# Performance work log

Hardware: AMD Instinct MI355X
Metric: run time of the kernel (lower is better)

Reference implementation:

```python
import jax, jax.numpy as jnp
import numpy as np

B, NQ = 4, 4096
HF, WF = 96, 96          # single-level feature map -> Nv = 9216
NV = HF * WF
E = 768                  # dim * num_frames = 192 * 4
NH, NP, NL = 8, 4, 1
HD = E // NH             # 96
EPS = 1e-6


def _layer_norm(x, w, b):
    m = jnp.mean(x, axis=-1, keepdims=True)
    v = jnp.var(x, axis=-1, keepdims=True)
    return (x - m) * jax.lax.rsqrt(v + EPS) * w + b


def _msda_core(value, shapes, loc, aw):
    # value: (B, Nv, H, D); loc: (B, Nq, H, L, P, 2) normalized in [0,1];
    # aw: (B, Nq, H, L, P). Bilinear sampling matching F.grid_sample
    # (align_corners=False, padding_mode='zeros'): pixel = loc * size - 0.5.
    Bn, Nv, H, D = value.shape
    Nq, P = loc.shape[1], loc.shape[4]
    out = jnp.zeros((Bn, H, Nq, D), value.dtype)
    start = 0
    for lvl in range(shapes.shape[0]):
        Hl, Wl = int(shapes[lvl, 0]), int(shapes[lvl, 1])
        v = value[:, start:start + Hl * Wl].transpose(0, 2, 1, 3)  # (B,H,S,D)
        start += Hl * Wl
        x = loc[:, :, :, lvl, :, 0] * Wl - 0.5  # (B,Nq,H,P)
        y = loc[:, :, :, lvl, :, 1] * Hl - 0.5
        x0, y0 = jnp.floor(x), jnp.floor(y)
        sampled = jnp.zeros((Bn, H, Nq, P, D), value.dtype)
        for dx in (0, 1):
            for dy in (0, 1):
                xi, yi = x0 + dx, y0 + dy
                w = (1.0 - jnp.abs(x - xi)) * (1.0 - jnp.abs(y - yi))
                valid = (xi >= 0) & (xi <= Wl - 1) & (yi >= 0) & (yi <= Hl - 1)
                idx = (jnp.clip(yi, 0, Hl - 1) * Wl
                       + jnp.clip(xi, 0, Wl - 1)).astype(jnp.int32)
                idx = idx.transpose(0, 2, 1, 3).reshape(Bn, H, Nq * P)
                g = jnp.take_along_axis(v, idx[..., None], axis=2)
                g = g.reshape(Bn, H, Nq, P, D)
                wz = jnp.where(valid, w, 0.0).transpose(0, 2, 1, 3)[..., None]
                sampled = sampled + g * wz
        awl = aw[:, :, :, lvl].transpose(0, 2, 1, 3)[..., None]  # (B,H,Nq,P,1)
        out = out + jnp.sum(sampled * awl, axis=3)
    return out.transpose(0, 2, 1, 3).reshape(Bn, Nq, H * D)


def setup_inputs():
    key = jax.random.key(0)
    ks = jax.random.split(key, 12)
    s = 0.02
    return {
        "query": jax.random.normal(ks[0], (B, NQ, E), jnp.float32),
        "reference_points": jax.random.uniform(ks[1], (B, NQ, NL, 2), jnp.float32),
        "feat": jax.random.normal(ks[2], (B, NV, E), jnp.float32),
        "spatial_shapes": jnp.array([[HF, WF]], jnp.int32),
        "level_start_index": jnp.zeros((NL,), jnp.int32),
        "ln_q_w": jnp.ones((E,), jnp.float32),
        "ln_q_b": jnp.zeros((E,), jnp.float32),
        "ln_f_w": jnp.ones((E,), jnp.float32),
        "ln_f_b": jnp.zeros((E,), jnp.float32),
        "W_value": jax.random.normal(ks[3], (E, E), jnp.float32) * s,
        "b_value": jnp.zeros((E,), jnp.float32),
        "W_off": jax.random.normal(ks[4], (E, NH * NL * NP * 2), jnp.float32) * s,
        "b_off": jax.random.normal(ks[5], (NH * NL * NP * 2,), jnp.float32) * s,
        "W_attn": jax.random.normal(ks[6], (E, NH * NL * NP), jnp.float32) * s,
        "b_attn": jnp.zeros((NH * NL * NP,), jnp.float32),
        "W_out": jax.random.normal(ks[7], (E, E), jnp.float32) * s,
        "b_out": jnp.zeros((E,), jnp.float32),
        "gamma": jax.random.normal(ks[8], (E,), jnp.float32) * s,
    }


def reference(query, reference_points, feat, spatial_shapes, level_start_index,
              ln_q_w, ln_q_b, ln_f_w, ln_f_b, W_value, b_value, W_off, b_off,
              W_attn, b_attn, W_out, b_out, gamma):
    shapes = np.asarray(spatial_shapes)  # static level shapes
    Bn, Nq, _ = query.shape
    Nv = feat.shape[1]
    q = _layer_norm(query, ln_q_w, ln_q_b)
    f = _layer_norm(feat, ln_f_w, ln_f_b)
    value = (f @ W_value + b_value).reshape(Bn, Nv, NH, HD)
    offsets = (q @ W_off + b_off).reshape(Bn, Nq, NH, NL, NP, 2)
    aw = jax.nn.softmax((q @ W_attn + b_attn).reshape(Bn, Nq, NH, NL * NP), -1)
    aw = aw.reshape(Bn, Nq, NH, NL, NP)
    # offset_normalizer = [W_l, H_l] per level
    norm = jnp.stack([jnp.asarray(shapes[:, 1], jnp.float32),
                      jnp.asarray(shapes[:, 0], jnp.float32)], axis=-1)  # (L,2)
    loc = (reference_points[:, :, None, :, None, :]
           + offsets / norm[None, None, None, :, None, :])
    out = _msda_core(value, shapes, loc, aw)
    out = out @ W_out + b_out
    attn = q + out  # mmcv MSDeformAttn adds identity (dropout=eval no-op)
    return query + gamma * attn
```

## Files before the change

### kernel.cpp

```cpp
#include <hip/hip_runtime.h>

#define BB     4
#define NQS    4096
#define NVS    9216
#define E_DIM  768
#define NHEAD  8
#define NPTS   4
#define HDIM   96
#define HFEAT  96
#define WFEAT  96
#define MQR    16384
#define NLNB   13312
#define NTRB   1152
#define NVALB  432
#define OROWS  64

typedef __attribute__((ext_vector_type(8))) short  s8v;
typedef __attribute__((ext_vector_type(4))) short  s4v;
typedef __attribute__((ext_vector_type(4))) float  f4v;

__device__ __forceinline__ unsigned short f2bf(float x) {
    unsigned int u = __builtin_bit_cast(unsigned int, x);
    unsigned int r = (u + 0x7fffu + ((u >> 16) & 1u)) >> 16;
    return (unsigned short)r;
}
__device__ __forceinline__ float bf2f(unsigned short s) {
    unsigned int u = ((unsigned int)s) << 16;
    return __builtin_bit_cast(float, u);
}
__device__ __forceinline__ float bf2f_s(short s) {
    return bf2f((unsigned short)s);
}

#define GLD16(gp, lp) \
    __builtin_amdgcn_global_load_lds( \
        (__attribute__((address_space(1))) void*)(gp), \
        (__attribute__((address_space(3))) void*)(lp), 16, 0, 0)

__global__ __launch_bounds__(256) void prep_kernel(
    const float* __restrict__ q, const float* __restrict__ f,
    const float* __restrict__ qw, const float* __restrict__ qb,
    const float* __restrict__ fw, const float* __restrict__ fb,
    unsigned short* __restrict__ qout, unsigned short* __restrict__ fout,
    float* __restrict__ stats,
    const float* __restrict__ W0, const float* __restrict__ W1,
    unsigned short* __restrict__ T0, unsigned short* __restrict__ T1,
    const float* __restrict__ W_off, const float* __restrict__ W_attn,
    const float* __restrict__ b_off, const float* __restrict__ b_attn,
    unsigned short* __restrict__ Wqc, float* __restrict__ bcat) {
    __shared__ float tile[32][33];
    const int bid = blockIdx.x;

    if (bid < NLNB) {
        const int wv = threadIdx.x >> 6, lane = threadIdx.x & 63;
        const int row = bid * 4 + wv;
        const bool isq = row < MQR;
        const float* x = isq ? (q + (size_t)row * E_DIM)
                             : (f + (size_t)(row - MQR) * E_DIM);
        const float4 v0 = ((const float4*)x)[lane];
        const float4 v1 = ((const float4*)x)[lane + 64];
        const float4 v2 = ((const float4*)x)[lane + 128];
        float s1 = v0.x + v0.y + v0.z + v0.w + v1.x + v1.y + v1.z + v1.w
                 + v2.x + v2.y + v2.z + v2.w;
        float s2 = v0.x * v0.x + v0.y * v0.y + v0.z * v0.z + v0.w * v0.w
                 + v1.x * v1.x + v1.y * v1.y + v1.z * v1.z + v1.w * v1.w
                 + v2.x * v2.x + v2.y * v2.y + v2.z * v2.z + v2.w * v2.w;
        #pragma unroll
        for (int o = 32; o > 0; o >>= 1) {
            s1 += __shfl_down(s1, o, 64);
            s2 += __shfl_down(s2, o, 64);
        }
        const float mean = __shfl(s1, 0, 64) * (1.0f / E_DIM);
        const float m2   = __shfl(s2, 0, 64) * (1.0f / E_DIM);
        const float rstd = rsqrtf(m2 - mean * mean + 1e-6f);
        if (isq && lane == 0) { stats[row * 2] = mean; stats[row * 2 + 1] = rstd; }
        const float* w = isq ? qw : fw;
        const float* b = isq ? qb : fb;
        unsigned short* o = isq ? (qout + (size_t)row * E_DIM)
                                : (fout + (size_t)(row - MQR) * E_DIM);
        const float4 vv[3] = {v0, v1, v2};
        #pragma unroll
        for (int c = 0; c < 3; c++) {
            const float4 w4 = ((const float4*)w)[lane + c * 64];
            const float4 b4 = ((const float4*)b)[lane + c * 64];
            s4v ov;
            ov[0] = (short)f2bf((vv[c].x - mean) * rstd * w4.x + b4.x);
            ov[1] = (short)f2bf((vv[c].y - mean) * rstd * w4.y + b4.y);
            ov[2] = (short)f2bf((vv[c].z - mean) * rstd * w4.z + b4.z);
            ov[3] = (short)f2bf((vv[c].w - mean) * rstd * w4.w + b4.w);
            ((s4v*)o)[lane + c * 64] = ov;
        }
    } else if (bid < NLNB + NTRB) {
        const int idx = bid - NLNB;
        const int z = idx / 576, r2 = idx - z * 576;
        const float* W = z ? W1 : W0;
        unsigned short* Wt = z ? T1 : T0;
        const int bi = (r2 / 24) * 32, bj = (r2 % 24) * 32;
        const int t = threadIdx.x;
        const int r = t >> 5, c = t & 31;
        #pragma unroll
        for (int i = 0; i < 4; i++)
            tile[r + i * 8][c] = W[(size_t)(bi + r + i * 8) * E_DIM + bj + c];
        __syncthreads();
        #pragma unroll
        for (int i = 0; i < 4; i++)
            Wt[(size_t)(bj + r + i * 8) * E_DIM + bi + c] = f2bf(tile[c][r + i * 8]);
    } else {
        const int idx = (bid - NLNB - NTRB) * 256 + threadIdx.x;
        const int rrow = idx / E_DIM, k = idx % E_DIM;
        float v = 0.f;
        if (rrow < 64) v = W_off[(size_t)k * 64 + rrow];
        else if (rrow < 96) v = W_attn[(size_t)k * 32 + (rrow - 64)];
        Wqc[idx] = f2bf(v);
        if (idx < 128) {
            float b = 0.f;
            if (idx < 64) b = b_off[idx];
            else if (idx < 96) b = b_attn[idx - 64];
            bcat[idx] = b;
        }
    }
}

template <int G>
__device__ __forceinline__ void tigroup(const unsigned short* as_, const s8v (&bfr)[2][4],
                                        f4v (&acc)[8][4], int quad, int l16, int wrow) {
    s8v af[2][2];
    #pragma unroll
    for (int c = 0; c < 2; c++)
        #pragma unroll
        for (int m = 0; m < 2; m++)
            af[c][m] = *(const s8v*)(as_ + ((size_t)((c * 4 + quad) * 256 + wrow * 128 + (G * 2 + m) * 16 + l16)) * 8);
    #pragma unroll
    for (int c = 0; c < 2; c++)
        #pragma unroll
        for (int m = 0; m < 2; m++)
            #pragma unroll
            for (int n = 0; n < 4; n++)
                acc[G * 2 + m][n] = __builtin_amdgcn_mfma_f32_16x16x32_bf16(
                    af[c][m], bfr[c][n], acc[G * 2 + m][n], 0, 0, 0);
}

__global__ __launch_bounds__(512, 2) void mfma_gemm256(
    const unsigned short* __restrict__ A, const unsigned short* __restrict__ Bt,
    const float* __restrict__ bias, unsigned short* __restrict__ C,
    const unsigned short* __restrict__ Aq, const unsigned short* __restrict__ Wqc,
    const float* __restrict__ bcat, float* __restrict__ offattn) {
    __shared__ unsigned short As[2][256 * 64];
    __shared__ unsigned short Bs[2][256 * 64];

    constexpr int K = E_DIM;
    constexpr int NT = K / 64;
    const int tid = threadIdx.x;
    const int wave = tid >> 6;
    const int lane = tid & 63;
    const int quad = lane >> 4;
    const int l16 = lane & 15;

    if (blockIdx.x < NVALB) {
        const int flat = blockIdx.x;
        const int cpx = NVALB >> 3;
        const int swz = (flat & 7) * cpx + (flat >> 3);
        const int bx = swz % 3;
        const int by = swz / 3;
        const int bm = by * 256;
        const int bn = bx * 256;
        const int wrow = wave >> 2;
        const int wcol = wave & 3;

        const unsigned short* gsrc[4][2];
        int ldst[4][2];
        #pragma unroll
        for (int h = 0; h < 4; h++) {
            #pragma unroll
            for (int i = 0; i < 2; i++) {
                const int ch = wave * 2 + i;
                const int s = ch >> 1, rsub = ch & 1;
                const int rw = (h & 1) * 128 + rsub * 64 + lane;
                const unsigned short* base = (h < 2) ? (A + (size_t)(bm + rw) * K)
                                                     : (Bt + (size_t)(bn + rw) * K);
                gsrc[h][i] = base + s * 8;
                ldst[h][i] = (s * 256 + rw) * 8;
            }
        }

        #define STAGE256(h, kt, buf) do { \
            unsigned short* lb_ = ((h) < 2 ? &As[(buf)][0] : &Bs[(buf)][0]); \
            GLD16(gsrc[h][0] + (size_t)(kt) * 64, lb_ + ldst[h][0]); \
            GLD16(gsrc[h][1] + (size_t)(kt) * 64, lb_ + ldst[h][1]); \
        } while (0)

        f4v acc[8][4] = {};

        #pragma unroll
        for (int h = 0; h < 4; h++) STAGE256(h, 0, 0);

        int cur = 0;
        for (int t = 0; t < NT; ++t) {
            const unsigned short* as_ = &As[cur][0];
            const unsigned short* bs_ = &Bs[cur][0];
            const int nb = cur ^ 1;
            const bool pf = (t + 1 < NT);

            if (pf) {
                STAGE256(0, t + 1, nb);
                asm volatile("s_waitcnt vmcnt(2)" ::: "memory");
            } else {
                asm volatile("s_waitcnt vmcnt(0)" ::: "memory");
            }
            __builtin_amdgcn_s_barrier();
            __builtin_amdgcn_sched_barrier(0);

            s8v bfr[2][4];
            #pragma unroll
            for (int c = 0; c < 2; c++)
                #pragma unroll
                for (int n = 0; n < 4; n++)
                    bfr[c][n] = *(const s8v*)(bs_ + ((size_t)((c * 4 + quad) * 256 + wcol * 64 + n * 16 + l16)) * 8);

            __builtin_amdgcn_s_setprio(1);
            tigroup<0>(as_, bfr, acc, quad, l16, wrow);
            __builtin_amdgcn_s_setprio(0);

            if (pf) STAGE256(1, t + 1, nb);
            __builtin_amdgcn_s_setprio(1);
            tigroup<1>(as_, bfr, acc, quad, l16, wrow);
            __builtin_amdgcn_s_setprio(0);

            if (pf) STAGE256(2, t + 1, nb);
            __builtin_amdgcn_s_setprio(1);
            tigroup<2>(as_, bfr, acc, quad, l16, wrow);
            __builtin_amdgcn_s_setprio(0);

            if (pf) STAGE256(3, t + 1, nb);
            s8v af3[2][2];
            #pragma unroll
            for (int c = 0; c < 2; c++)
                #pragma unroll
                for (int m = 0; m < 2; m++)
                    af3[c][m] = *(const s8v*)(as_ + ((size_t)((c * 4 + quad) * 256 + wrow * 128 + (6 + m) * 16 + l16)) * 8);
            asm volatile("s_waitcnt lgkmcnt(0)" ::: "memory");
            __builtin_amdgcn_sched_barrier(0);
            __builtin_amdgcn_s_barrier();
            __builtin_amdgcn_sched_barrier(0);
            __builtin_amdgcn_s_setprio(1);
            #pragma unroll
            for (int c = 0; c < 2; c++)
                #pragma unroll
                for (int m = 0; m < 2; m++)
                    #pragma unroll
                    for (int n = 0; n < 4; n++)
                        acc[6 + m][n] = __builtin_amdgcn_mfma_f32_16x16x32_bf16(
                            af3[c][m], bfr[c][n], acc[6 + m][n], 0, 0, 0);
            __builtin_amdgcn_s_setprio(0);

            cur ^= 1;
        }
        #undef STAGE256

        #pragma unroll
        for (int ti = 0; ti < 8; ti++) {
            const int gm_base = bm + wrow * 128 + ti * 16 + quad * 4;
            #pragma unroll
            for (int tj = 0; tj < 4; tj++) {
                const int gn = bn + wcol * 64 + tj * 16 + l16;
                const float bv = bias[gn];
                const int hh = gn / HDIM, dd = gn - hh * HDIM;
                #pragma unroll
                for (int r = 0; r < 4; r++) {
                    const int gm = gm_base + r;
                    const float v = acc[ti][tj][r] + bv;
                    const int b = gm / NVS, s = gm - b * NVS;
                    const size_t vidx = (((size_t)b * NHEAD + hh) * NVS + s) * HDIM + dd;
                    C[vidx] = f2bf(v);
                }
            }
        }
    } else {
        const int bm = (blockIdx.x - NVALB) * 128;
        const int wrow = wave >> 2;
        const int wcol = wave & 3;
        unsigned short* As0 = &As[0][0];
        unsigned short* Bs0 = &Bs[0][0];

        const unsigned short* arow[2];
        const unsigned short* brow[2];
        int loff[2];
        #pragma unroll
        for (int i = 0; i < 2; i++) {
            const int ch = wave * 2 + i;
            const int s = ch >> 1, r = (ch & 1) * 64 + lane;
            arow[i] = Aq + (size_t)(bm + r) * K + s * 8;
            brow[i] = Wqc + (size_t)r * K + s * 8;
            loff[i] = (s * 128 + r) * 8;
        }

        f4v accq[4][2] = {};

        for (int k0 = 0; k0 < K; k0 += 64) {
            #pragma unroll
            for (int i = 0; i < 2; i++) GLD16(arow[i] + k0, As0 + loff[i]);
            #pragma unroll
            for (int i = 0; i < 2; i++) GLD16(brow[i] + k0, Bs0 + loff[i]);

            __syncthreads();

            #pragma unroll
            for (int c = 0; c < 2; c++) {
                s8v af[4], bf[2];
                #pragma unroll
                for (int m = 0; m < 4; m++)
                    af[m] = *(const s8v*)(As0 + ((size_t)((c * 4 + quad) * 128 + wrow * 64 + m * 16 + l16)) * 8);
                #pragma unroll
                for (int n = 0; n < 2; n++)
                    bf[n] = *(const s8v*)(Bs0 + ((size_t)((c * 4 + quad) * 128 + wcol * 32 + n * 16 + l16)) * 8);
                #pragma unroll
                for (int m = 0; m < 4; m++)
                    #pragma unroll
                    for (int n = 0; n < 2; n++)
                        accq[m][n] = __builtin_amdgcn_mfma_f32_16x16x32_bf16(af[m], bf[n], accq[m][n], 0, 0, 0);
            }
            __syncthreads();
        }

        #pragma unroll
        for (int m = 0; m < 4; m++) {
            const int gm_base = bm + wrow * 64 + m * 16 + quad * 4;
            #pragma unroll
            for (int n = 0; n < 2; n++) {
                const int gn = wcol * 32 + n * 16 + l16;
                const float bv = bcat[gn];
                #pragma unroll
                for (int r = 0; r < 4; r++)
                    offattn[(size_t)(gm_base + r) * 128 + gn] = accq[m][n][r] + bv;
            }
        }
    }
}

__global__ __launch_bounds__(512, 2) void msda_oproj_kernel(
    const unsigned short* __restrict__ value,
    const float* __restrict__ oa,
    const float* __restrict__ refp,
    const unsigned short* __restrict__ Wo,
    const float* __restrict__ bias,
    const float* __restrict__ query, const float* __restrict__ qstats,
    const float* __restrict__ lnw, const float* __restrict__ lnb,
    const float* __restrict__ gamma, float* __restrict__ out) {
    __shared__ unsigned short Ams[OROWS * E_DIM];

    const int bid = blockIdx.x;
    const int swzb = (bid & 7) * (256 >> 3) + (bid >> 3);
    const int row0 = swzb * OROWS;
    const int t = threadIdx.x;
    const int b = row0 >> 12;

    #pragma unroll
    for (int it = 0; it < 12; ++it) {
        const int tt = it * 512 + t;
        const int r = tt / 96;
        const int rem = tt - r * 96;
        const int h = rem / 12;
        const int j = rem - h * 12;
        const int row = row0 + r;
        const float* oar = oa + (size_t)row * 128;
        float a0 = oar[64 + h * 4 + 0], a1 = oar[64 + h * 4 + 1];
        float a2 = oar[64 + h * 4 + 2], a3 = oar[64 + h * 4 + 3];
        float mx = fmaxf(fmaxf(a0, a1), fmaxf(a2, a3));
        float e0 = __expf(a0 - mx), e1 = __expf(a1 - mx);
        float e2 = __expf(a2 - mx), e3 = __expf(a3 - mx);
        float inv = 1.0f / (e0 + e1 + e2 + e3);
        const float aww[4] = {e0 * inv, e1 * inv, e2 * inv, e3 * inv};
        const float rx = refp[(size_t)row * 2 + 0] * WFEAT - 0.5f;
        const float ry = refp[(size_t)row * 2 + 1] * HFEAT - 0.5f;
        const unsigned short* vb = value + ((size_t)(b * NHEAD + h) * NVS) * HDIM + j * 8;

        float acc[8] = {};
        #pragma unroll
        for (int p = 0; p < 4; p++) {
            const float x = rx + oar[h * 8 + p * 2 + 0];
            const float y = ry + oar[h * 8 + p * 2 + 1];
            const float aw = aww[p];
            const float x0f = floorf(x), y0f = floorf(y);
            const float fx = x - x0f, fy = y - y0f;
            const int ix0 = (int)x0f, iy0 = (int)y0f;
            const int ix1 = ix0 + 1, iy1 = iy0 + 1;
            const float wx0 = (ix0 >= 0 && ix0 < WFEAT) ? (1.f - fx) : 0.f;
            const float wx1 = (ix1 >= 0 && ix1 < WFEAT) ? fx : 0.f;
            const float wy0 = (iy0 >= 0 && iy0 < HFEAT) ? (1.f - fy) : 0.f;
            const float wy1 = (iy1 >= 0 && iy1 < HFEAT) ? fy : 0.f;
            const int cx0 = min(max(ix0, 0), WFEAT - 1);
            const int cx1 = min(max(ix1, 0), WFEAT - 1);
            const int cy0 = min(max(iy0, 0), HFEAT - 1);
            const int cy1 = min(max(iy1, 0), HFEAT - 1);
            const float w00 = aw * wy0 * wx0, w01 = aw * wy0 * wx1;
            const float w10 = aw * wy1 * wx0, w11 = aw * wy1 * wx1;
            const s8v v00 = *(const s8v*)(vb + (size_t)(cy0 * WFEAT + cx0) * HDIM);
            const s8v v01 = *(const s8v*)(vb + (size_t)(cy0 * WFEAT + cx1) * HDIM);
            const s8v v10 = *(const s8v*)(vb + (size_t)(cy1 * WFEAT + cx0) * HDIM);
            const s8v v11 = *(const s8v*)(vb + (size_t)(cy1 * WFEAT + cx1) * HDIM);
            #pragma unroll
            for (int k = 0; k < 8; k++) {
                acc[k] += w00 * bf2f_s(v00[k]) + w01 * bf2f_s(v01[k])
                        + w10 * bf2f_s(v10[k]) + w11 * bf2f_s(v11[k]);
            }
        }
        s8v o;
        #pragma unroll
        for (int k = 0; k < 8; k++) o[k] = (short)f2bf(acc[k]);
        const int col16 = (h * 12 + j) ^ (r & 7);
        *(s8v*)(&Ams[((size_t)r * 96 + col16) * 8]) = o;
    }
    __syncthreads();

    const int wave = t >> 6;
    const int lane = t & 63;
    const int quad = lane >> 4;
    const int l16 = lane & 15;

    const unsigned short* bcol[6];
    #pragma unroll
    for (int n = 0; n < 6; n++)
        bcol[n] = Wo + (size_t)(wave * 96 + n * 16 + l16) * E_DIM + quad * 8;

    f4v acc[4][6] = {};

    for (int k0 = 0; k0 < E_DIM; k0 += 32) {
        const int kc = (k0 >> 3) + quad;
        s8v af[4], bf[6];
        #pragma unroll
        for (int m = 0; m < 4; m++) {
            const int r = m * 16 + l16;
            af[m] = *(const s8v*)(&Ams[((size_t)r * 96 + (kc ^ (r & 7))) * 8]);
        }
        #pragma unroll
        for (int n = 0; n < 6; n++)
            bf[n] = *(const s8v*)(bcol[n] + k0);
        #pragma unroll
        for (int m = 0; m < 4; m++)
            #pragma unroll
            for (int n = 0; n < 6; n++)
                acc[m][n] = __builtin_amdgcn_mfma_f32_16x16x32_bf16(af[m], bf[n], acc[m][n], 0, 0, 0);
    }

    #pragma unroll
    for (int m = 0; m < 4; m++) {
        const int gm_base = row0 + m * 16 + quad * 4;
        #pragma unroll
        for (int n = 0; n < 6; n++) {
            const int gn = wave * 96 + n * 16 + l16;
            const float bv = bias[gn];
            #pragma unroll
            for (int r = 0; r < 4; r++) {
                const int gm = gm_base + r;
                const size_t idx = (size_t)gm * E_DIM + gn;
                const float qv = query[idx];
                const float qln = (qv - qstats[gm * 2]) * qstats[gm * 2 + 1] * lnw[gn] + lnb[gn];
                out[idx] = qv + gamma[gn] * (qln + acc[m][n][r] + bv);
            }
        }
    }
}

extern "C" void kernel_launch(void* const* d_in, const int* in_sizes, int n_in,
                              void* d_out, int out_size, void* d_ws, size_t ws_size,
                              hipStream_t stream) {
    (void)in_sizes; (void)n_in; (void)out_size; (void)ws_size;

    const float* query  = (const float*)d_in[0];
    const float* refp   = (const float*)d_in[1];
    const float* feat   = (const float*)d_in[2];
    const float* ln_q_w = (const float*)d_in[5];
    const float* ln_q_b = (const float*)d_in[6];
    const float* ln_f_w = (const float*)d_in[7];
    const float* ln_f_b = (const float*)d_in[8];
    const float* W_val  = (const float*)d_in[9];
    const float* b_val  = (const float*)d_in[10];
    const float* W_off  = (const float*)d_in[11];
    const float* b_off  = (const float*)d_in[12];
    const float* W_attn = (const float*)d_in[13];
    const float* b_attn = (const float*)d_in[14];
    const float* W_out  = (const float*)d_in[15];
    const float* b_out  = (const float*)d_in[16];
    const float* gamma  = (const float*)d_in[17];
    float* out = (float*)d_out;

    const int MQ = BB * NQS;
    const int MV = BB * NVS;

    char* ws = (char*)d_ws;
    float*          q_stats = (float*)(ws + 0);
    unsigned short* qbf     = (unsigned short*)(ws + 131072);
    unsigned short* fbf     = (unsigned short*)(ws + 25296896);
    unsigned short* val_bf  = (unsigned short*)(ws + 81920000);
    float*          offattn = (float*)(ws + 163708928);
    unsigned short* Wv_t    = (unsigned short*)(ws + 172097536);
    unsigned short* Wo_t    = (unsigned short*)(ws + 173277184);
    unsigned short* Wqc_t   = (unsigned short*)(ws + 174456832);
    float*          bcat    = (float*)(ws + 174653440);

    prep_kernel<<<NLNB + NTRB + 384, 256, 0, stream>>>(
        query, feat, ln_q_w, ln_q_b, ln_f_w, ln_f_b, qbf, fbf, q_stats,
        W_val, W_out, Wv_t, Wo_t, W_off, W_attn, b_off, b_attn, Wqc_t, bcat);

    mfma_gemm256<<<NVALB + 128, 512, 0, stream>>>(
        fbf, Wv_t, b_val, val_bf, qbf, Wqc_t, bcat, offattn);

    msda_oproj_kernel<<<MQ / OROWS, 512, 0, stream>>>(
        val_bf, offattn, refp, Wo_t, b_out, query, q_stats, ln_q_w, ln_q_b,
        gamma, out);
}
```

Baseline: 411.7 us.

## Fuse offset/attention projection GEMM into sampling kernel, drop offattn buffer

Moves the query offset/attention-logit projection (16384x768x128) out of the value-GEMM launch and into the MSDA+output-projection kernel. Each block computes its 64x128 slice with MFMA directly from global bf16 memory into a new shared buffer. This removes the global offattn round trip and the heterogeneous extra blocks in the value GEMM, which now uses a uniform 2D grid. In exchange the sampling kernel uses 32KB more LDS and does an unstaged global-load GEMM before sampling, which may lower occupancy and add latency.

Result: slower. 436.1 us (+5.9%).

```diff
diff --git a/kernel.cpp b/kernel.cpp
--- a/kernel.cpp
+++ b/kernel.cpp
@@ -12,7 +12,6 @@
 #define MQR    16384
 #define NLNB   13312
 #define NTRB   1152
-#define NVALB  432
 #define OROWS  64
 
 typedef __attribute__((ext_vector_type(8))) short  s8v;
@@ -142,9 +141,7 @@
 
 __global__ __launch_bounds__(512, 2) void mfma_gemm256(
     const unsigned short* __restrict__ A, const unsigned short* __restrict__ Bt,
-    const float* __restrict__ bias, unsigned short* __restrict__ C,
-    const unsigned short* __restrict__ Aq, const unsigned short* __restrict__ Wqc,
-    const float* __restrict__ bcat, float* __restrict__ offattn) {
+    const float* __restrict__ bias, unsigned short* __restrict__ C) {
     __shared__ unsigned short As[2][256 * 64];
     __shared__ unsigned short Bs[2][256 * 64];
 
@@ -156,182 +153,122 @@
     const int quad = lane >> 4;
     const int l16 = lane & 15;
 
-    if (blockIdx.x < NVALB) {
-        const int flat = blockIdx.x;
-        const int cpx = NVALB >> 3;
-        const int swz = (flat & 7) * cpx + (flat >> 3);
-        const int bx = swz % 3;
-        const int by = swz / 3;
-        const int bm = by * 256;
-        const int bn = bx * 256;
-        const int wrow = wave >> 2;
-        const int wcol = wave & 3;
-
-        const unsigned short* gsrc[4][2];
-        int ldst[4][2];
-        #pragma unroll
-        for (int h = 0; h < 4; h++) {
-            #pragma unroll
-            for (int i = 0; i < 2; i++) {
-                const int ch = wave * 2 + i;
-                const int s = ch >> 1, rsub = ch & 1;
-                const int rw = (h & 1) * 128 + rsub * 64 + lane;
-                const unsigned short* base = (h < 2) ? (A + (size_t)(bm + rw) * K)
-                                                     : (Bt + (size_t)(bn + rw) * K);
-                gsrc[h][i] = base + s * 8;
-                ldst[h][i] = (s * 256 + rw) * 8;
-            }
-        }
-
-        #define STAGE256(h, kt, buf) do { \
-            unsigned short* lb_ = ((h) < 2 ? &As[(buf)][0] : &Bs[(buf)][0]); \
-            GLD16(gsrc[h][0] + (size_t)(kt) * 64, lb_ + ldst[h][0]); \
-            GLD16(gsrc[h][1] + (size_t)(kt) * 64, lb_ + ldst[h][1]); \
-        } while (0)
-
-        f4v acc[8][4] = {};
-
-        #pragma unroll
-        for (int h = 0; h < 4; h++) STAGE256(h, 0, 0);
-
-        int cur = 0;
-        for (int t = 0; t < NT; ++t) {
-            const unsigned short* as_ = &As[cur][0];
-            const unsigned short* bs_ = &Bs[cur][0];
-            const int nb = cur ^ 1;
-            const bool pf = (t + 1 < NT);
-
-            if (pf) {
-                STAGE256(0, t + 1, nb);
-                asm volatile("s_waitcnt vmcnt(2)" ::: "memory");
-            } else {
-                asm volatile("s_waitcnt vmcnt(0)" ::: "memory");
-            }
-            __builtin_amdgcn_s_barrier();
-            __builtin_amdgcn_sched_barrier(0);
-
-            s8v bfr[2][4];
-            #pragma unroll
-            for (int c = 0; c < 2; c++)
+    const int nwg = gridDim.x * gridDim.y;
+    const int flat = blockIdx.y * gridDim.x + blockIdx.x;
+    const int cpx = nwg >> 3;
+    const int swz = (flat & 7) * cpx + (flat >> 3);
+    const int bx = swz % gridDim.x;
+    const int by = swz / gridDim.x;
+    const int bm = by * 256;
+    const int bn = bx * 256;
+    const int wrow = wave >> 2;
+    const int wcol = wave & 3;
+
+    const unsigned short* gsrc[4][2];
+    int ldst[4][2];
+    #pragma unroll
+    for (int h = 0; h < 4; h++) {
+        #pragma unroll
+        for (int i = 0; i < 2; i++) {
+            const int ch = wave * 2 + i;
+            const int s = ch >> 1, rsub = ch & 1;
+            const int rw = (h & 1) * 128 + rsub * 64 + lane;
+            const unsigned short* base = (h < 2) ? (A + (size_t)(bm + rw) * K)
+                                                 : (Bt + (size_t)(bn + rw) * K);
+            gsrc[h][i] = base + s * 8;
+            ldst[h][i] = (s * 256 + rw) * 8;
+        }
+    }
+
+    #define STAGE256(h, kt, buf) do { \
+        unsigned short* lb_ = ((h) < 2 ? &As[(buf)][0] : &Bs[(buf)][0]); \
+        GLD16(gsrc[h][0] + (size_t)(kt) * 64, lb_ + ldst[h][0]); \
+        GLD16(gsrc[h][1] + (size_t)(kt) * 64, lb_ + ldst[h][1]); \
+    } while (0)
+
+    f4v acc[8][4] = {};
+
+    #pragma unroll
+    for (int h = 0; h < 4; h++) STAGE256(h, 0, 0);
+
+    int cur = 0;
+    for (int t = 0; t < NT; ++t) {
+        const unsigned short* as_ = &As[cur][0];
+        const unsigned short* bs_ = &Bs[cur][0];
+        const int nb = cur ^ 1;
+        const bool pf = (t + 1 < NT);
+
+        if (pf) {
+            STAGE256(0, t + 1, nb);
+            asm volatile("s_waitcnt vmcnt(2)" ::: "memory");
+        } else {
+            asm volatile("s_waitcnt vmcnt(0)" ::: "memory");
+        }
+        __builtin_amdgcn_s_barrier();
+        __builtin_amdgcn_sched_barrier(0);
+
+        s8v bfr[2][4];
+        #pragma unroll
+        for (int c = 0; c < 2; c++)
+            #pragma unroll
+            for (int n = 0; n < 4; n++)
+                bfr[c][n] = *(const s8v*)(bs_ + ((size_t)((c * 4 + quad) * 256 + wcol * 64 + n * 16 + l16)) * 8);
+
+        __builtin_amdgcn_s_setprio(1);
+        tigroup<0>(as_, bfr, acc, quad, l16, wrow);
+        __builtin_amdgcn_s_setprio(0);
+
+        if (pf) STAGE256(1, t + 1, nb);
+        __builtin_amdgcn_s_setprio(1);
+        tigroup<1>(as_, bfr, acc, quad, l16, wrow);
+        __builtin_amdgcn_s_setprio(0);
+
+        if (pf) STAGE256(2, t + 1, nb);
+        __builtin_amdgcn_s_setprio(1);
+        tigroup<2>(as_, bfr, acc, quad, l16, wrow);
+        __builtin_amdgcn_s_setprio(0);
+
+        if (pf) STAGE256(3, t + 1, nb);
+        s8v af3[2][2];
+        #pragma unroll
+        for (int c = 0; c < 2; c++)
+            #pragma unroll
+            for (int m = 0; m < 2; m++)
+                af3[c][m] = *(const s8v*)(as_ + ((size_t)((c * 4 + quad) * 256 + wrow * 128 + (6 + m) * 16 + l16)) * 8);
+        asm volatile("s_waitcnt lgkmcnt(0)" ::: "memory");
+        __builtin_amdgcn_sched_barrier(0);
+        __builtin_amdgcn_s_barrier();
+        __builtin_amdgcn_sched_barrier(0);
+        __builtin_amdgcn_s_setprio(1);
+        #pragma unroll
+        for (int c = 0; c < 2; c++)
+            #pragma unroll
+            for (int m = 0; m < 2; m++)
                 #pragma unroll
                 for (int n = 0; n < 4; n++)
-                    bfr[c][n] = *(const s8v*)(bs_ + ((size_t)((c * 4 + quad) * 256 + wcol * 64 + n * 16 + l16)) * 8);
-
-            __builtin_amdgcn_s_setprio(1);
-            tigroup<0>(as_, bfr, acc, quad, l16, wrow);
-            __builtin_amdgcn_s_setprio(0);
-
-            if (pf) STAGE256(1, t + 1, nb);
-            __builtin_amdgcn_s_setprio(1);
-            tigroup<1>(as_, bfr, acc, quad, l16, wrow);
-            __builtin_amdgcn_s_setprio(0);
-
-            if (pf) STAGE256(2, t + 1, nb);
-            __builtin_amdgcn_s_setprio(1);
-            tigroup<2>(as_, bfr, acc, quad, l16, wrow);
-            __builtin_amdgcn_s_setprio(0);
-
-            if (pf) STAGE256(3, t + 1, nb);
-            s8v af3[2][2];
-            #pragma unroll
-            for (int c = 0; c < 2; c++)
-                #pragma unroll
-                for (int m = 0; m < 2; m++)
-                    af3[c][m] = *(const s8v*)(as_ + ((size_t)((c * 4 + quad) * 256 + wrow * 128 + (6 + m) * 16 + l16)) * 8);
-            asm volatile("s_waitcnt lgkmcnt(0)" ::: "memory");
-            __builtin_amdgcn_sched_barrier(0);
-            __builtin_amdgcn_s_barrier();
-            __builtin_amdgcn_sched_barrier(0);
-            __builtin_amdgcn_s_setprio(1);
-            #pragma unroll
-            for (int c = 0; c < 2; c++)
-                #pragma unroll
-                for (int m = 0; m < 2; m++)
-                    #pragma unroll
-                    for (int n = 0; n < 4; n++)
-                        acc[6 + m][n] = __builtin_amdgcn_mfma_f32_16x16x32_bf16(
-                            af3[c][m], bfr[c][n], acc[6 + m][n], 0, 0, 0);
-            __builtin_amdgcn_s_setprio(0);
-
-            cur ^= 1;
-        }
-        #undef STAGE256
-
-        #pragma unroll
-        for (int ti = 0; ti < 8; ti++) {
-            const int gm_base = bm + wrow * 128 + ti * 16 + quad * 4;
-            #pragma unroll
-            for (int tj = 0; tj < 4; tj++) {
-                const int gn = bn + wcol * 64 + tj * 16 + l16;
-                const float bv = bias[gn];
-                const int hh = gn / HDIM, dd = gn - hh * HDIM;
-                #pragma unroll
-                for (int r = 0; r < 4; r++) {
-                    const int gm = gm_base + r;
-                    const float v = acc[ti][tj][r] + bv;
-                    const int b = gm / NVS, s = gm - b * NVS;
-                    const size_t vidx = (((size_t)b * NHEAD + hh) * NVS + s) * HDIM + dd;
-                    C[vidx] = f2bf(v);
-                }
-            }
-        }
-    } else {
-        const int bm = (blockIdx.x - NVALB) * 128;
-        const int wrow = wave >> 2;
-        const int wcol = wave & 3;
-        unsigned short* As0 = &As[0][0];
-        unsigned short* Bs0 = &Bs[0][0];
-
-        const unsigned short* arow[2];
-        const unsigned short* brow[2];
-        int loff[2];
-        #pragma unroll
-        for (int i = 0; i < 2; i++) {
-            const int ch = wave * 2 + i;
-            const int s = ch >> 1, r = (ch & 1) * 64 + lane;
-            arow[i] = Aq + (size_t)(bm + r) * K + s * 8;
-            brow[i] = Wqc + (size_t)r * K + s * 8;
-            loff[i] = (s * 128 + r) * 8;
-        }
-
-        f4v accq[4][2] = {};
-
-        for (int k0 = 0; k0 < K; k0 += 64) {
-            #pragma unroll
-            for (int i = 0; i < 2; i++) GLD16(arow[i] + k0, As0 + loff[i]);
-            #pragma unroll
-            for (int i = 0; i < 2; i++) GLD16(brow[i] + k0, Bs0 + loff[i]);
-
-            __syncthreads();
-
-            #pragma unroll
-            for (int c = 0; c < 2; c++) {
-                s8v af[4], bf[2];
-                #pragma unroll
-                for (int m = 0; m < 4; m++)
-                    af[m] = *(const s8v*)(As0 + ((size_t)((c * 4 + quad) * 128 + wrow * 64 + m * 16 + l16)) * 8);
-                #pragma unroll
-                for (int n = 0; n < 2; n++)
-                    bf[n] = *(const s8v*)(Bs0 + ((size_t)((c * 4 + quad) * 128 + wcol * 32 + n * 16 + l16)) * 8);
-                #pragma unroll
-                for (int m = 0; m < 4; m++)
-                    #pragma unroll
-                    for (int n = 0; n < 2; n++)
-                        accq[m][n] = __builtin_amdgcn_mfma_f32_16x16x32_bf16(af[m], bf[n], accq[m][n], 0, 0, 0);
-            }
-            __syncthreads();
-        }
-
-        #pragma unroll
-        for (int m = 0; m < 4; m++) {
-            const int gm_base = bm + wrow * 64 + m * 16 + quad * 4;
-            #pragma unroll
-            for (int n = 0; n < 2; n++) {
-                const int gn = wcol * 32 + n * 16 + l16;
-                const float bv = bcat[gn];
-                #pragma unroll
-                for (int r = 0; r < 4; r++)
-                    offattn[(size_t)(gm_base + r) * 128 + gn] = accq[m][n][r] + bv;
+                    acc[6 + m][n] = __builtin_amdgcn_mfma_f32_16x16x32_bf16(
+                        af3[c][m], bfr[c][n], acc[6 + m][n], 0, 0, 0);
+        __builtin_amdgcn_s_setprio(0);
+
+        cur ^= 1;
+    }
+    #undef STAGE256
+
+    #pragma unroll
+    for (int ti = 0; ti < 8; ti++) {
+        const int gm_base = bm + wrow * 128 + ti * 16 + quad * 4;
+        #pragma unroll
+        for (int tj = 0; tj < 4; tj++) {
+            const int gn = bn + wcol * 64 + tj * 16 + l16;
+            const float bv = bias[gn];
+            const int hh = gn / HDIM, dd = gn - hh * HDIM;
+            #pragma unroll
+            for (int r = 0; r < 4; r++) {
+                const int gm = gm_base + r;
+                const float v = acc[ti][tj][r] + bv;
+                const int b = gm / NVS, s = gm - b * NVS;
+                const size_t vidx = (((size_t)b * NHEAD + hh) * NVS + s) * HDIM + dd;
+                C[vidx] = f2bf(v);
             }
         }
     }
@@ -339,7 +276,9 @@
 
 __global__ __launch_bounds__(512, 2) void msda_oproj_kernel(
     const unsigned short* __restrict__ value,
-    const float* __restrict__ oa,
+    const unsigned short* __restrict__ qbf,
+    const unsigned short* __restrict__ Wqc,
+    const float* __restrict__ bcat,
     const float* __restrict__ refp,
     const unsigned short* __restrict__ Wo,
     const float* __restrict__ bias,
@@ -347,12 +286,45 @@
     const float* __restrict__ lnw, const float* __restrict__ lnb,
     const float* __restrict__ gamma, float* __restrict__ out) {
     __shared__ unsigned short Ams[OROWS * E_DIM];
+    __shared__ float off_s[OROWS * 128];
 
     const int bid = blockIdx.x;
     const int swzb = (bid & 7) * (256 >> 3) + (bid >> 3);
     const int row0 = swzb * OROWS;
     const int t = threadIdx.x;
     const int b = row0 >> 12;
+
+    const int wave = t >> 6;
+    const int lane = t & 63;
+    const int quad = lane >> 4;
+    const int l16 = lane & 15;
+
+    {
+        const unsigned short* arow[4];
+        #pragma unroll
+        for (int ti = 0; ti < 4; ti++)
+            arow[ti] = qbf + (size_t)(row0 + ti * 16 + l16) * E_DIM + quad * 8;
+        const unsigned short* brow = Wqc + (size_t)(wave * 16 + l16) * E_DIM + quad * 8;
+
+        f4v a4[4] = {};
+        #pragma unroll
+        for (int k0 = 0; k0 < E_DIM; k0 += 32) {
+            const s8v bf = *(const s8v*)(brow + k0);
+            #pragma unroll
+            for (int ti = 0; ti < 4; ti++) {
+                const s8v af = *(const s8v*)(arow[ti] + k0);
+                a4[ti] = __builtin_amdgcn_mfma_f32_16x16x32_bf16(af, bf, a4[ti], 0, 0, 0);
+            }
+        }
+        const int col = wave * 16 + l16;
+        const float bv = bcat[col];
+        #pragma unroll
+        for (int ti = 0; ti < 4; ti++)
+            #pragma unroll
+            for (int r = 0; r < 4; r++)
+                off_s[(ti * 16 + quad * 4 + r) * 128 + col] = a4[ti][r] + bv;
+    }
+    __syncthreads();
 
     #pragma unroll
     for (int it = 0; it < 12; ++it) {
@@ -362,7 +334,7 @@
         const int h = rem / 12;
         const int j = rem - h * 12;
         const int row = row0 + r;
-        const float* oar = oa + (size_t)row * 128;
+        const float* oar = off_s + r * 128;
         float a0 = oar[64 + h * 4 + 0], a1 = oar[64 + h * 4 + 1];
         float a2 = oar[64 + h * 4 + 2], a3 = oar[64 + h * 4 + 3];
         float mx = fmaxf(fmaxf(a0, a1), fmaxf(a2, a3));
@@ -412,11 +384,6 @@
     }
     __syncthreads();
 
-    const int wave = t >> 6;
-    const int lane = t & 63;
-    const int quad = lane >> 4;
-    const int l16 = lane & 15;
-
     const unsigned short* bcol[6];
     #pragma unroll
     for (int n = 0; n < 6; n++)
@@ -492,7 +459,6 @@
     unsigned short* qbf     = (unsigned short*)(ws + 131072);
     unsigned short* fbf     = (unsigned short*)(ws + 25296896);
     unsigned short* val_bf  = (unsigned short*)(ws + 81920000);
-    float*          offattn = (float*)(ws + 163708928);
     unsigned short* Wv_t    = (unsigned short*)(ws + 172097536);
     unsigned short* Wo_t    = (unsigned short*)(ws + 173277184);
     unsigned short* Wqc_t   = (unsigned short*)(ws + 174456832);
@@ -502,10 +468,10 @@
         query, feat, ln_q_w, ln_q_b, ln_f_w, ln_f_b, qbf, fbf, q_stats,
         W_val, W_out, Wv_t, Wo_t, W_off, W_attn, b_off, b_attn, Wqc_t, bcat);
 
-    mfma_gemm256<<<NVALB + 128, 512, 0, stream>>>(
-        fbf, Wv_t, b_val, val_bf, qbf, Wqc_t, bcat, offattn);
+    mfma_gemm256<<<dim3(E_DIM / 256, MV / 256), 512, 0, stream>>>(
+        fbf, Wv_t, b_val, val_bf);
 
     msda_oproj_kernel<<<MQ / OROWS, 512, 0, stream>>>(
-        val_bf, offattn, refp, Wo_t, b_out, query, q_stats, ln_q_w, ln_q_b,
-        gamma, out);
-}
+        val_bf, qbf, Wqc_t, bcat, refp, Wo_t, b_out, query, q_stats,
+        ln_q_w, ln_q_b, gamma, out);
+}
```
